# Optimization experiments

Measured on AMD Instinct MI355X. Metric: run time of the kernel, lower is better.

The kernel has to match this reference:

```python
import jax, jax.numpy as jnp
import numpy as np

N = 8192      # batch_size * length
B = 8
K = 30
D = 320       # hidden_nf = input_nf = output_nf
EPS = 1e-8
DIST_W = 1.0


def setup_inputs() -> dict:
    key = jax.random.key(0)
    k1, k2, k3, k4, k5, k6, k7 = jax.random.split(key, 7)
    h = jax.random.normal(k1, (N, D), dtype=jnp.float32)
    coord = jax.random.normal(k2, (N, 3), dtype=jnp.float32)
    # row: each node repeated K times (fixed-k neighborhood grouping implied by reshape(B,-1,K))
    row = jnp.repeat(jnp.arange(N, dtype=jnp.int64), K)
    col = jax.random.randint(k3, (N * K,), 0, N, dtype=jnp.int64)
    edge_index = jnp.stack([row, col], axis=0)
    # node_mlp params: Linear(2D -> D), SiLU, Linear(D -> D)
    s1 = 1.0 / np.sqrt(2 * D)
    s2 = 1.0 / np.sqrt(D)
    W1 = jax.random.uniform(k4, (2 * D, D), jnp.float32, -s1, s1)
    b1 = jax.random.uniform(k5, (D,), jnp.float32, -s1, s1)
    W2 = jax.random.uniform(k6, (D, D), jnp.float32, -s2, s2)
    b2 = jax.random.uniform(k7, (D,), jnp.float32, -s2, s2)
    return {"h": h, "coord": coord, "W1": W1, "b1": b1, "W2": W2, "b2": b2,
            "edge_index": edge_index, "batch_size": B, "k": K}


def reference(h, coord, W1, b1, W2, b2, edge_index, batch_size, k):
    row, col = edge_index[0], edge_index[1]
    d = h.shape[-1]
    # coord2radial (normalize=False)
    coord_diff = coord[row] - coord[col]                      # [E,3]
    radial = jnp.sum(coord_diff ** 2, axis=1, keepdims=True)  # [E,1]
    # edge_model: dot-product attention fused with inverse-distance score
    src, tgt = h[row], h[col]                                 # [E,D]
    attn = jnp.sum(src * tgt, axis=-1).reshape(batch_size, -1, k)   # [B,L,K]
    dist_score = (1.0 / (radial + EPS)).reshape(batch_size, -1, k)  # [B,L,K]
    attn_score = jax.nn.softmax(attn + DIST_W * dist_score, axis=-1)[..., None]  # [B,L,K,1]
    edge_feat = tgt.reshape(batch_size, -1, k, d) * attn_score       # [B,L,K,D]
    # coord_model (coords_agg='mean')
    trans = coord_diff.reshape(batch_size, -1, k, 3) * attn_score    # [B,L,K,3]
    coord_out = coord + jnp.mean(trans, axis=2).reshape(-1, 3)
    # node_model (residual=True)
    agg = jnp.sum(edge_feat, axis=2).reshape(-1, d)                  # [N,D]
    z = jnp.concatenate([h, agg], axis=1)                            # [N,2D]
    out = jax.nn.silu(z @ W1 + b1) @ W2 + b2
    h_out = h + out
    return (h_out, coord_out)
```

## Files before the change

kernel.cpp:

```cpp
#include <hip/hip_runtime.h>
#include <hip/hip_bf16.h>
#include <math.h>

#define DHID 320
#define KNN  30

typedef float f4    __attribute__((ext_vector_type(4)));
typedef float f32x4 __attribute__((ext_vector_type(4)));
typedef short bf16x8 __attribute__((ext_vector_type(8)));
typedef short bf16x4 __attribute__((ext_vector_type(4)));

static __device__ __forceinline__ short f2bf(float x) {
    union { float f; unsigned u; } v; v.f = x;
    unsigned r = v.u + 0x7FFFu + ((v.u >> 16) & 1u);
    return (short)(r >> 16);
}

__global__ __launch_bounds__(256)
void edge_kernel(const float* __restrict__ h,
                 const float* __restrict__ coord,
                 const int*   __restrict__ col,
                 short*       __restrict__ aggb,
                 float*       __restrict__ coord_out,
                 int N)
{
    int wid  = (int)((blockIdx.x * 256u + threadIdx.x) >> 6);
    int lane = threadIdx.x & 63;
    if (wid >= N) return;

    const float* hi = h + (size_t)wid * DHID;
    f4    hv = *(const f4*)(hi + 4 * lane);
    float ht = hi[256 + lane];

    float cx = coord[3 * wid + 0];
    float cy = coord[3 * wid + 1];
    float cz = coord[3 * wid + 2];

    const int* cp = col + (size_t)wid * KNN;
    int jv = (lane < KNN) ? cp[lane] : 0;
    float pjx = 0.f, pjy = 0.f, pjz = 0.f;
    if (lane < KNN) {
        pjx = coord[3 * jv + 0];
        pjy = coord[3 * jv + 1];
        pjz = coord[3 * jv + 2];
    }

    float run_m = -INFINITY, run_l = 0.f;
    f4    accv = {0.f, 0.f, 0.f, 0.f};
    float acct = 0.f;
    float ax = 0.f, ay = 0.f, az = 0.f;

#pragma unroll 2
    for (int k = 0; k < KNN; ++k) {
        int j = __shfl(jv, k);
        const float* hj = h + (size_t)j * DHID;
        f4    gv = *(const f4*)(hj + 4 * lane);
        float gt = hj[256 + lane];

        float dot = hv[0] * gv[0];
        dot = fmaf(hv[1], gv[1], dot);
        dot = fmaf(hv[2], gv[2], dot);
        dot = fmaf(hv[3], gv[3], dot);
        dot = fmaf(ht, gt, dot);
#pragma unroll
        for (int off = 32; off; off >>= 1) dot += __shfl_xor(dot, off);

        float dx = cx - __shfl(pjx, k);
        float dy = cy - __shfl(pjy, k);
        float dz = cz - __shfl(pjz, k);
        float radial = dx * dx + dy * dy + dz * dz;
        float s = dot + 1.0f / (radial + 1e-8f);

        float nm = fmaxf(run_m, s);
        float sc = __expf(run_m - nm);
        float w  = __expf(s - nm);
        run_l = run_l * sc + w;
        accv  = accv * sc + w * gv;
        acct  = acct * sc + w * gt;
        ax = ax * sc + w * dx;
        ay = ay * sc + w * dy;
        az = az * sc + w * dz;
        run_m = nm;
    }

    float inv = 1.0f / run_l;
    short* ao = aggb + (size_t)wid * DHID;
    bf16x4 o;
#pragma unroll
    for (int i = 0; i < 4; ++i) o[i] = f2bf(accv[i] * inv);
    *(bf16x4*)(ao + 4 * lane) = o;
    ao[256 + lane] = f2bf(acct * inv);

    if (lane == 0) {
        float s = inv / (float)KNN;
        coord_out[3 * wid + 0] = cx + ax * s;
        coord_out[3 * wid + 1] = cy + ay * s;
        coord_out[3 * wid + 2] = cz + az * s;
    }
}

__global__ __launch_bounds__(256)
void wconv_kernel(const float* __restrict__ W1, const float* __restrict__ W2,
                  short* __restrict__ Wt1, short* __restrict__ Wt2)
{
    int i = blockIdx.x * 256 + threadIdx.x;
    if (i < 640 * 320) {
        int k = i / 320, c = i - k * 320;
        int tile = c >> 4, lr = c & 15;
        int t = k >> 5, kg = (k >> 3) & 3, j = k & 7;
        Wt1[(size_t)tile * (20 * 512) + t * 512 + kg * 128 + lr * 8 + j] = f2bf(W1[i]);
    } else {
        int q = i - 640 * 320;
        int k = q / 320, c = q - k * 320;
        int tile = c >> 4, lr = c & 15;
        int t = k >> 5, kg = (k >> 3) & 3, j = k & 7;
        Wt2[(size_t)tile * (10 * 512) + t * 512 + kg * 128 + lr * 8 + j] = f2bf(W2[q]);
    }
}

__global__ __launch_bounds__(256)
void mlp_fused_kernel(const float* __restrict__ h,
                      const short* __restrict__ aggb,
                      const short* __restrict__ Wt1,
                      const short* __restrict__ Wt2,
                      const float* __restrict__ b1,
                      const float* __restrict__ b2,
                      float*       __restrict__ hout)
{
    __shared__ short zs[16 * 640];
    __shared__ short h1s[16 * 320];

    const int tid  = threadIdx.x;
    const int lane = tid & 63;
    const int wv   = tid >> 6;
    const int lrow = lane & 15;
    const int kg   = lane >> 4;
    const int r0   = blockIdx.x * 16;

    for (int c = tid; c < 1280; c += 256) {
        int row = c / 80;
        int zc  = (c - row * 80) * 8;
        int sw  = (row & 7) << 4;
        bf16x8 v;
        if (zc < DHID) {
            const float* hp = h + (size_t)(r0 + row) * DHID + zc;
            f4 lo = *(const f4*)hp;
            f4 hi = *(const f4*)(hp + 4);
#pragma unroll
            for (int j = 0; j < 4; ++j) { v[j] = f2bf(lo[j]); v[4 + j] = f2bf(hi[j]); }
        } else {
            v = *(const bf16x8*)(aggb + (size_t)(r0 + row) * DHID + (zc - DHID));
        }
        *(bf16x8*)((char*)zs + ((row * 1280 + zc * 2) ^ sw)) = v;
    }
    __syncthreads();

    const int   sw    = (lrow & 7) << 4;
    const char* abase = (const char*)zs + lrow * 1280;

    f32x4 acc[5] = {};
    {
        const short* B = Wt1 + (size_t)(wv * 5) * (20 * 512) + kg * 128 + lrow * 8;
        for (int t = 0; t < 20; ++t) {
            bf16x8 a = *(const bf16x8*)(abase + ((t * 64 + kg * 16) ^ sw));
#pragma unroll
            for (int i = 0; i < 5; ++i) {
                bf16x8 b = *(const bf16x8*)(B + (size_t)i * (20 * 512) + t * 512);
                acc[i] = __builtin_amdgcn_mfma_f32_16x16x32_bf16(a, b, acc[i], 0, 0, 0);
            }
        }
    }

#pragma unroll
    for (int i = 0; i < 5; ++i) {
        int colc = (wv * 5 + i) * 16 + lrow;
        float bb = b1[colc];
#pragma unroll
        for (int r = 0; r < 4; ++r) {
            int row = kg * 4 + r;
            float x = acc[i][r] + bb;
            x = x / (1.f + __expf(-x));
            *(short*)((char*)h1s + ((row * 640 + colc * 2) ^ ((row & 7) << 4))) = f2bf(x);
        }
    }
    __syncthreads();

    f32x4 acc2[5] = {};
    {
        const short* B = Wt2 + (size_t)(wv * 5) * (10 * 512) + kg * 128 + lrow * 8;
        const char* a2base = (const char*)h1s + lrow * 640;
        for (int t = 0; t < 10; ++t) {
            bf16x8 a = *(const bf16x8*)(a2base + ((t * 64 + kg * 16) ^ sw));
#pragma unroll
            for (int i = 0; i < 5; ++i) {
                bf16x8 b = *(const bf16x8*)(B + (size_t)i * (10 * 512) + t * 512);
                acc2[i] = __builtin_amdgcn_mfma_f32_16x16x32_bf16(a, b, acc2[i], 0, 0, 0);
            }
        }
    }

#pragma unroll
    for (int i = 0; i < 5; ++i) {
        int colc = (wv * 5 + i) * 16 + lrow;
        float bb = b2[colc];
#pragma unroll
        for (int r = 0; r < 4; ++r) {
            int grow = r0 + kg * 4 + r;
            hout[(size_t)grow * DHID + colc] =
                acc2[i][r] + bb + h[(size_t)grow * DHID + colc];
        }
    }
}

extern "C" void kernel_launch(void* const* d_in, const int* in_sizes, int n_in,
                              void* d_out, int out_size, void* d_ws, size_t ws_size,
                              hipStream_t stream)
{
    const float* h     = (const float*)d_in[0];
    const float* coord = (const float*)d_in[1];
    const float* W1    = (const float*)d_in[2];
    const float* b1    = (const float*)d_in[3];
    const float* W2    = (const float*)d_in[4];
    const float* b2    = (const float*)d_in[5];
    const int*   ei    = (const int*)d_in[6];

    const int N  = in_sizes[0] / DHID;
    const int NK = N * KNN;

    float* out       = (float*)d_out;
    float* hout      = out;
    float* coord_out = out + (size_t)N * DHID;

    short* aggb = (short*)d_ws;
    short* Wt1  = aggb + (size_t)N * DHID;
    short* Wt2  = Wt1 + 20 * 20 * 512;

    const int* col = ei + NK;

    edge_kernel<<<N / 4, 256, 0, stream>>>(h, coord, col, aggb, coord_out, N);
    wconv_kernel<<<(640 * 320 + 320 * 320) / 256, 256, 0, stream>>>(W1, W2, Wt1, Wt2);
    mlp_fused_kernel<<<N / 16, 256, 0, stream>>>(h, aggb, Wt1, Wt2, b1, b2, hout);
}
```

Baseline: 135.3 us.

## Pre-convert h to bf16 for neighbor gathers and use 32-row MLP tiles

```diff
diff --git a/kernel.cpp b/kernel.cpp
--- a/kernel.cpp
+++ b/kernel.cpp
@@ -15,9 +15,39 @@
     unsigned r = v.u + 0x7FFFu + ((v.u >> 16) & 1u);
     return (short)(r >> 16);
 }
+static __device__ __forceinline__ float bf2f(short s) {
+    union { float f; unsigned u; } v;
+    v.u = ((unsigned)(unsigned short)s) << 16;
+    return v.f;
+}
+
+__global__ __launch_bounds__(256)
+void conv_kernel(const float* __restrict__ W1, const float* __restrict__ W2,
+                 const float* __restrict__ h,
+                 short* __restrict__ Wt1, short* __restrict__ Wt2,
+                 short* __restrict__ hb, int N)
+{
+    int i = blockIdx.x * 256 + threadIdx.x;
+    if (i < 640 * 320) {
+        int k = i / 320, c = i - k * 320;
+        int tile = c >> 4, lr = c & 15;
+        int t = k >> 5, kg = (k >> 3) & 3, j = k & 7;
+        Wt1[(size_t)tile * (20 * 512) + t * 512 + kg * 128 + lr * 8 + j] = f2bf(W1[i]);
+    } else if (i < 640 * 320 + 320 * 320) {
+        int q = i - 640 * 320;
+        int k = q / 320, c = q - k * 320;
+        int tile = c >> 4, lr = c & 15;
+        int t = k >> 5, kg = (k >> 3) & 3, j = k & 7;
+        Wt2[(size_t)tile * (10 * 512) + t * 512 + kg * 128 + lr * 8 + j] = f2bf(W2[q]);
+    } else {
+        int q = i - (640 * 320 + 320 * 320);
+        if (q < N * DHID) hb[q] = f2bf(h[q]);
+    }
+}
 
 __global__ __launch_bounds__(256)
 void edge_kernel(const float* __restrict__ h,
+                 const short* __restrict__ hb,
                  const float* __restrict__ coord,
                  const int*   __restrict__ col,
                  short*       __restrict__ aggb,
@@ -53,9 +83,10 @@
 #pragma unroll 2
     for (int k = 0; k < KNN; ++k) {
         int j = __shfl(jv, k);
-        const float* hj = h + (size_t)j * DHID;
-        f4    gv = *(const f4*)(hj + 4 * lane);
-        float gt = hj[256 + lane];
+        const short* hj = hb + (size_t)j * DHID;
+        bf16x4 gb = *(const bf16x4*)(hj + 4 * lane);
+        float  gt = bf2f(hj[256 + lane]);
+        f4 gv = { bf2f(gb[0]), bf2f(gb[1]), bf2f(gb[2]), bf2f(gb[3]) };
 
         float dot = hv[0] * gv[0];
         dot = fmaf(hv[1], gv[1], dot);
@@ -99,27 +130,9 @@
     }
 }
 
-__global__ __launch_bounds__(256)
-void wconv_kernel(const float* __restrict__ W1, const float* __restrict__ W2,
-                  short* __restrict__ Wt1, short* __restrict__ Wt2)
-{
-    int i = blockIdx.x * 256 + threadIdx.x;
-    if (i < 640 * 320) {
-        int k = i / 320, c = i - k * 320;
-        int tile = c >> 4, lr = c & 15;
-        int t = k >> 5, kg = (k >> 3) & 3, j = k & 7;
-        Wt1[(size_t)tile * (20 * 512) + t * 512 + kg * 128 + lr * 8 + j] = f2bf(W1[i]);
-    } else {
-        int q = i - 640 * 320;
-        int k = q / 320, c = q - k * 320;
-        int tile = c >> 4, lr = c & 15;
-        int t = k >> 5, kg = (k >> 3) & 3, j = k & 7;
-        Wt2[(size_t)tile * (10 * 512) + t * 512 + kg * 128 + lr * 8 + j] = f2bf(W2[q]);
-    }
-}
-
-__global__ __launch_bounds__(256)
+__global__ __launch_bounds__(512)
 void mlp_fused_kernel(const float* __restrict__ h,
+                      const short* __restrict__ hb,
                       const short* __restrict__ aggb,
                       const short* __restrict__ Wt1,
                       const short* __restrict__ Wt2,
@@ -127,27 +140,25 @@
                       const float* __restrict__ b2,
                       float*       __restrict__ hout)
 {
-    __shared__ short zs[16 * 640];
-    __shared__ short h1s[16 * 320];
+    __shared__ short zs[32 * 640];
+    __shared__ short h1s[32 * 320];
 
     const int tid  = threadIdx.x;
     const int lane = tid & 63;
     const int wv   = tid >> 6;
+    const int rt   = wv & 1;
+    const int cs   = wv >> 1;
     const int lrow = lane & 15;
     const int kg   = lane >> 4;
-    const int r0   = blockIdx.x * 16;
-
-    for (int c = tid; c < 1280; c += 256) {
+    const int r0   = blockIdx.x * 32;
+
+    for (int c = tid; c < 2560; c += 512) {
         int row = c / 80;
         int zc  = (c - row * 80) * 8;
         int sw  = (row & 7) << 4;
         bf16x8 v;
         if (zc < DHID) {
-            const float* hp = h + (size_t)(r0 + row) * DHID + zc;
-            f4 lo = *(const f4*)hp;
-            f4 hi = *(const f4*)(hp + 4);
-#pragma unroll
-            for (int j = 0; j < 4; ++j) { v[j] = f2bf(lo[j]); v[4 + j] = f2bf(hi[j]); }
+            v = *(const bf16x8*)(hb + (size_t)(r0 + row) * DHID + zc);
         } else {
             v = *(const bf16x8*)(aggb + (size_t)(r0 + row) * DHID + (zc - DHID));
         }
@@ -156,11 +167,11 @@
     __syncthreads();
 
     const int   sw    = (lrow & 7) << 4;
-    const char* abase = (const char*)zs + lrow * 1280;
+    const char* abase = (const char*)zs + (rt * 16 + lrow) * 1280;
 
     f32x4 acc[5] = {};
     {
-        const short* B = Wt1 + (size_t)(wv * 5) * (20 * 512) + kg * 128 + lrow * 8;
+        const short* B = Wt1 + (size_t)(cs * 5) * (20 * 512) + kg * 128 + lrow * 8;
         for (int t = 0; t < 20; ++t) {
             bf16x8 a = *(const bf16x8*)(abase + ((t * 64 + kg * 16) ^ sw));
 #pragma unroll
@@ -173,11 +184,11 @@
 
 #pragma unroll
     for (int i = 0; i < 5; ++i) {
-        int colc = (wv * 5 + i) * 16 + lrow;
+        int colc = (cs * 5 + i) * 16 + lrow;
         float bb = b1[colc];
 #pragma unroll
         for (int r = 0; r < 4; ++r) {
-            int row = kg * 4 + r;
+            int row = rt * 16 + kg * 4 + r;
             float x = acc[i][r] + bb;
             x = x / (1.f + __expf(-x));
             *(short*)((char*)h1s + ((row * 640 + colc * 2) ^ ((row & 7) << 4))) = f2bf(x);
@@ -187,8 +198,8 @@
 
     f32x4 acc2[5] = {};
     {
-        const short* B = Wt2 + (size_t)(wv * 5) * (10 * 512) + kg * 128 + lrow * 8;
-        const char* a2base = (const char*)h1s + lrow * 640;
+        const short* B = Wt2 + (size_t)(cs * 5) * (10 * 512) + kg * 128 + lrow * 8;
+        const char* a2base = (const char*)h1s + (rt * 16 + lrow) * 640;
         for (int t = 0; t < 10; ++t) {
             bf16x8 a = *(const bf16x8*)(a2base + ((t * 64 + kg * 16) ^ sw));
 #pragma unroll
@@ -201,11 +212,11 @@
 
 #pragma unroll
     for (int i = 0; i < 5; ++i) {
-        int colc = (wv * 5 + i) * 16 + lrow;
+        int colc = (cs * 5 + i) * 16 + lrow;
         float bb = b2[colc];
 #pragma unroll
         for (int r = 0; r < 4; ++r) {
-            int grow = r0 + kg * 4 + r;
+            int grow = r0 + rt * 16 + kg * 4 + r;
             hout[(size_t)grow * DHID + colc] =
                 acc2[i][r] + bb + h[(size_t)grow * DHID + colc];
         }
@@ -234,10 +245,12 @@
     short* aggb = (short*)d_ws;
     short* Wt1  = aggb + (size_t)N * DHID;
     short* Wt2  = Wt1 + 20 * 20 * 512;
+    short* hb   = Wt2 + 20 * 10 * 512;
 
     const int* col = ei + NK;
 
-    edge_kernel<<<N / 4, 256, 0, stream>>>(h, coord, col, aggb, coord_out, N);
-    wconv_kernel<<<(640 * 320 + 320 * 320) / 256, 256, 0, stream>>>(W1, W2, Wt1, Wt2);
-    mlp_fused_kernel<<<N / 16, 256, 0, stream>>>(h, aggb, Wt1, Wt2, b1, b2, hout);
-}
+    const int conv_elems = 640 * 320 + 320 * 320 + N * DHID;
+    conv_kernel<<<(conv_elems + 255) / 256, 256, 0, stream>>>(W1, W2, h, Wt1, Wt2, hb, N);
+    edge_kernel<<<N / 4, 256, 0, stream>>>(h, hb, coord, col, aggb, coord_out, N);
+    mlp_fused_kernel<<<N / 32, 512, 0, stream>>>(h, hb, aggb, Wt1, Wt2, b1, b2, hout);
+}
```

Result: no change. 137.3 us (+1.5%).
